# Kernel optimization log

Measured on AMD Instinct MI355X. Metric: run time of the kernel, lower is better.

The kernel has to match this reference:

```python
import jax, jax.numpy as jnp
import numpy as np

THRESH = 0.9   # config['thresh_cnn']
R = 2          # config['radius'] -> maxpool kernel 2R+1=5, stride 1, padding R


def setup_inputs() -> dict:
    key = jax.random.key(0)
    # [B=1, C=1, D=64, H=512, W=512]
    pred_vol = jax.random.uniform(key, (1, 1, 64, 512, 512), dtype=jnp.float32)
    return {"pred_vol": pred_vol}


def reference(pred_vol):
    # threshold: keep values > thresh, else 0
    pred_thresh = jnp.where(pred_vol > THRESH, pred_vol, 0.0)
    # 3D max-pool, kernel 2R+1, stride 1, padding R (torch pads with -inf for maxpool)
    k = 2 * R + 1
    mp = jax.lax.reduce_window(
        pred_thresh, -jnp.inf, jax.lax.max,
        window_dimensions=(1, 1, k, k, k),
        window_strides=(1, 1, 1, 1, 1),
        padding=[(0, 0), (0, 0), (R, R), (R, R), (R, R)],
    )
    # keep only strict local maxima of the thresholded volume
    conf_vol = jnp.where((mp > 0.0) & (mp == pred_thresh), mp, 0.0)
    return jnp.squeeze(conf_vol)  # [D, H, W] dense peak confidence map
```

## Files before the change

### kernel.cpp

```cpp
#include <hip/hip_runtime.h>


#define THRESH 0.9f

constexpr int D = 64, H = 512, W = 512;
constexpr int HW = H * W;
constexpr int TW = 64;
constexpr int TH = 16;
constexpr int DCHUNK = 16;
constexpr int HALO = 2;
constexpr int LROWS = TH + 2 * HALO;
constexpr int WMC = 16;
constexpr int WM_S = WMC + 1;
constexpr int CEN_S = 17;
constexpr int NS = DCHUNK + 2 * HALO;

typedef float floatx4 __attribute__((ext_vector_type(4)));

__device__ __forceinline__ void barrier_no_drain() {
    asm volatile("s_waitcnt lgkmcnt(0)\n\ts_barrier" ::: "memory");
}

__device__ __forceinline__ float4 max4(float4 a, float4 b) {
    return make_float4(fmaxf(a.x, b.x), fmaxf(a.y, b.y),
                       fmaxf(a.z, b.z), fmaxf(a.w, b.w));
}

__device__ __forceinline__ float4 wmax5(float4 a, float4 b, float4 c) {
    const float f2 = a.z, f3 = a.w, f4 = b.x, f5 = b.y, f6 = b.z, f7 = b.w;
    const float f8 = c.x, f9 = c.y;
    const float m45 = fmaxf(f4, f5);
    const float m56 = fmaxf(f5, f6);
    const float m345 = fmaxf(f3, m45);
    const float m456 = fmaxf(f4, m56);
    const float m567 = fmaxf(m56, f7);
    const float m678 = fmaxf(fmaxf(f6, f7), f8);
    float4 r;
    r.x = fmaxf(fmaxf(f2, f6), m345);
    r.y = fmaxf(fmaxf(f3, f7), m456);
    r.z = fmaxf(fmaxf(f4, f8), m567);
    r.w = fmaxf(fmaxf(f5, f9), m678);
    return r;
}

__global__ __launch_bounds__(256)
void peak3d_kernel(const float* __restrict__ in, float* __restrict__ out) {
    __shared__ float4 wm [2][LROWS * WM_S];
    __shared__ float4 cen[2][TH * CEN_S];

    const int tx = threadIdx.x;
    const int ty = threadIdx.y;
    const int tid = ty * 16 + tx;

    const int w0 = blockIdx.x * TW;
    const int h0 = blockIdx.y * TH;
    const int d0 = blockIdx.z * DCHUNK;

    const int rA = tid >> 4, cA = (tid & 15) + 1;
    const bool hasB = (tid < 64);
    const int rB = 16 + (tid >> 4);
    const int cB = cA;

    const int ghA = h0 + rA - HALO;
    const int ghB = h0 + rB - HALO;
    const bool vAr_ = (unsigned)ghA < (unsigned)H;
    const bool vBr_ = hasB && ((unsigned)ghB < (unsigned)H);
    const int gwl = w0 + 4 * cA - 8;
    const int gwm = w0 + 4 * cA - 4;
    const int gwr = w0 + 4 * cA;
    const bool vl = (unsigned)gwl < (unsigned)W;
    const bool vr = (unsigned)gwr < (unsigned)W;
    const size_t offAl = (size_t)(vAr_ ? ghA : 0) * W + (vl ? gwl : 0);
    const size_t offAm = (size_t)(vAr_ ? ghA : 0) * W + gwm;
    const size_t offAr = (size_t)(vAr_ ? ghA : 0) * W + (vr ? gwr : 0);
    const size_t offBl = (size_t)(vBr_ ? ghB : 0) * W + (vl ? gwl : 0);
    const size_t offBm = (size_t)(vBr_ ? ghB : 0) * W + gwm;
    const size_t offBr = (size_t)(vBr_ ? ghB : 0) * W + (vr ? gwr : 0);
    const bool vAl = vAr_ && vl, vAm = vAr_, vArr = vAr_ && vr;
    const bool vBl = vBr_ && vl, vBm = vBr_, vBrr = vBr_ && vr;

    const float4 zero4 = make_float4(0.f, 0.f, 0.f, 0.f);
    float4 win[5], cen_r[3];
#pragma unroll
    for (int k = 0; k < 5; ++k) win[k] = zero4;
#pragma unroll
    for (int k = 0; k < 3; ++k) cen_r[k] = zero4;

    auto ld4 = [&](size_t off) {
        return *reinterpret_cast<const float4*>(in + off);
    };
    auto loadStage = [&](int dd, float4* pf) {
#pragma unroll
        for (int i = 0; i < 6; ++i) pf[i] = zero4;
        if (dd >= 0 && dd < D) {
            const size_t sb = (size_t)dd * HW;
            if (vAl)  pf[0] = ld4(sb + offAl);
            if (vAm)  pf[1] = ld4(sb + offAm);
            if (vArr) pf[2] = ld4(sb + offAr);
            if (vBl)  pf[3] = ld4(sb + offBl);
            if (vBm)  pf[4] = ld4(sb + offBm);
            if (vBrr) pf[5] = ld4(sb + offBr);
        }
    };

    float4 pf[6];
    loadStage(d0 - HALO, pf);

#pragma unroll
    for (int t = 0; t < NS; ++t) {
        const int buf = t & 1;

        {
            const float4 wA = wmax5(pf[0], pf[1], pf[2]);
            wm[buf][rA * WM_S + (cA - 1)] = wA;
            if (rA >= HALO)
                cen[buf][(rA - HALO) * CEN_S + (cA - 1)] = pf[1];
            if (hasB) {
                const float4 wB = wmax5(pf[3], pf[4], pf[5]);
                wm[buf][rB * WM_S + (cB - 1)] = wB;
                if (rB <= TH + HALO - 1)
                    cen[buf][(rB - HALO) * CEN_S + (cB - 1)] = pf[4];
            }
        }
        if (t + 1 < NS) loadStage(d0 - HALO + t + 1, pf);

        barrier_no_drain();

        {
            const float4* wp = &wm[buf][ty * WM_S + tx];
            const float4 hv = max4(max4(max4(wp[0 * WM_S], wp[1 * WM_S]),
                                        max4(wp[3 * WM_S], wp[4 * WM_S])),
                                   wp[2 * WM_S]);
            win[t % 5] = hv;
            cen_r[t % 3] = cen[buf][ty * CEN_S + tx];
        }

        if (t >= 4) {
            const int dout = d0 + (t - 4);
            const float4 mp = max4(max4(max4(win[0], win[1]),
                                        max4(win[2], win[3])), win[4]);
            const float4 c = cen_r[(t + 1) % 3];
            floatx4 res;
            res.x = (c.x > THRESH && mp.x == c.x) ? c.x : 0.f;
            res.y = (c.y > THRESH && mp.y == c.y) ? c.y : 0.f;
            res.z = (c.z > THRESH && mp.z == c.z) ? c.z : 0.f;
            res.w = (c.w > THRESH && mp.w == c.w) ? c.w : 0.f;
            floatx4* op = reinterpret_cast<floatx4*>(
                out + (size_t)dout * HW + (size_t)(h0 + ty) * W + (w0 + 4 * tx));
            __builtin_nontemporal_store(res, op);
        }
    }
}

extern "C" void kernel_launch(void* const* d_in, const int* in_sizes, int n_in,
                              void* d_out, int out_size, void* d_ws, size_t ws_size,
                              hipStream_t stream) {
    const float* in = (const float*)d_in[0];
    float* out = (float*)d_out;
    dim3 grid(W / TW, H / TH, D / DCHUNK);
    dim3 block(16, 16, 1);
    hipLaunchKernelGGL(peak3d_kernel, grid, block, 0, stream, in, out);
}
```

Measured before the change: 117.0 us.

## Use 320-thread blocks with one halo row per thread and halve depth chunk

```diff
diff --git a/kernel.cpp b/kernel.cpp
--- a/kernel.cpp
+++ b/kernel.cpp
@@ -7,11 +7,10 @@
 constexpr int HW = H * W;
 constexpr int TW = 64;
 constexpr int TH = 16;
-constexpr int DCHUNK = 16;
+constexpr int DCHUNK = 8;
 constexpr int HALO = 2;
 constexpr int LROWS = TH + 2 * HALO;
-constexpr int WMC = 16;
-constexpr int WM_S = WMC + 1;
+constexpr int WM_S = 17;
 constexpr int CEN_S = 17;
 constexpr int NS = DCHUNK + 2 * HALO;
 
@@ -43,41 +42,29 @@
     return r;
 }
 
-__global__ __launch_bounds__(256)
+__global__ __launch_bounds__(320, 8)
 void peak3d_kernel(const float* __restrict__ in, float* __restrict__ out) {
     __shared__ float4 wm [2][LROWS * WM_S];
     __shared__ float4 cen[2][TH * CEN_S];
 
     const int tx = threadIdx.x;
     const int ty = threadIdx.y;
-    const int tid = ty * 16 + tx;
 
     const int w0 = blockIdx.x * TW;
     const int h0 = blockIdx.y * TH;
     const int d0 = blockIdx.z * DCHUNK;
 
-    const int rA = tid >> 4, cA = (tid & 15) + 1;
-    const bool hasB = (tid < 64);
-    const int rB = 16 + (tid >> 4);
-    const int cB = cA;
-
-    const int ghA = h0 + rA - HALO;
-    const int ghB = h0 + rB - HALO;
-    const bool vAr_ = (unsigned)ghA < (unsigned)H;
-    const bool vBr_ = hasB && ((unsigned)ghB < (unsigned)H);
-    const int gwl = w0 + 4 * cA - 8;
-    const int gwm = w0 + 4 * cA - 4;
-    const int gwr = w0 + 4 * cA;
-    const bool vl = (unsigned)gwl < (unsigned)W;
-    const bool vr = (unsigned)gwr < (unsigned)W;
-    const size_t offAl = (size_t)(vAr_ ? ghA : 0) * W + (vl ? gwl : 0);
-    const size_t offAm = (size_t)(vAr_ ? ghA : 0) * W + gwm;
-    const size_t offAr = (size_t)(vAr_ ? ghA : 0) * W + (vr ? gwr : 0);
-    const size_t offBl = (size_t)(vBr_ ? ghB : 0) * W + (vl ? gwl : 0);
-    const size_t offBm = (size_t)(vBr_ ? ghB : 0) * W + gwm;
-    const size_t offBr = (size_t)(vBr_ ? ghB : 0) * W + (vr ? gwr : 0);
-    const bool vAl = vAr_ && vl, vAm = vAr_, vArr = vAr_ && vr;
-    const bool vBl = vBr_ && vl, vBm = vBr_, vBrr = vBr_ && vr;
+    const int gh  = h0 + ty - HALO;
+    const bool vR = (unsigned)gh < (unsigned)H;
+    const int gwl = w0 + 4 * tx - 4;
+    const int gwm = w0 + 4 * tx;
+    const int gwr = w0 + 4 * tx + 4;
+    const bool vl = vR && (gwl >= 0);
+    const bool vr = vR && (gwr < W);
+    const size_t rbase = (size_t)(vR ? gh : 0) * W;
+    const size_t offl = rbase + (gwl >= 0 ? gwl : 0);
+    const size_t offm = rbase + gwm;
+    const size_t offr = rbase + (gwr < W ? gwr : 0);
 
     const float4 zero4 = make_float4(0.f, 0.f, 0.f, 0.f);
     float4 win[5], cen_r[3];
@@ -90,64 +77,53 @@
         return *reinterpret_cast<const float4*>(in + off);
     };
     auto loadStage = [&](int dd, float4* pf) {
-#pragma unroll
-        for (int i = 0; i < 6; ++i) pf[i] = zero4;
+        pf[0] = zero4; pf[1] = zero4; pf[2] = zero4;
         if (dd >= 0 && dd < D) {
             const size_t sb = (size_t)dd * HW;
-            if (vAl)  pf[0] = ld4(sb + offAl);
-            if (vAm)  pf[1] = ld4(sb + offAm);
-            if (vArr) pf[2] = ld4(sb + offAr);
-            if (vBl)  pf[3] = ld4(sb + offBl);
-            if (vBm)  pf[4] = ld4(sb + offBm);
-            if (vBrr) pf[5] = ld4(sb + offBr);
+            if (vl) pf[0] = ld4(sb + offl);
+            if (vR) pf[1] = ld4(sb + offm);
+            if (vr) pf[2] = ld4(sb + offr);
         }
     };
 
-    float4 pf[6];
+    float4 pf[3];
     loadStage(d0 - HALO, pf);
 
 #pragma unroll
     for (int t = 0; t < NS; ++t) {
         const int buf = t & 1;
 
-        {
-            const float4 wA = wmax5(pf[0], pf[1], pf[2]);
-            wm[buf][rA * WM_S + (cA - 1)] = wA;
-            if (rA >= HALO)
-                cen[buf][(rA - HALO) * CEN_S + (cA - 1)] = pf[1];
-            if (hasB) {
-                const float4 wB = wmax5(pf[3], pf[4], pf[5]);
-                wm[buf][rB * WM_S + (cB - 1)] = wB;
-                if (rB <= TH + HALO - 1)
-                    cen[buf][(rB - HALO) * CEN_S + (cB - 1)] = pf[4];
-            }
-        }
+        wm[buf][ty * WM_S + tx] = wmax5(pf[0], pf[1], pf[2]);
+        if (ty >= HALO && ty < TH + HALO)
+            cen[buf][(ty - HALO) * CEN_S + tx] = pf[1];
+
         if (t + 1 < NS) loadStage(d0 - HALO + t + 1, pf);
 
         barrier_no_drain();
 
-        {
+        if (ty < TH) {
             const float4* wp = &wm[buf][ty * WM_S + tx];
             const float4 hv = max4(max4(max4(wp[0 * WM_S], wp[1 * WM_S]),
                                         max4(wp[3 * WM_S], wp[4 * WM_S])),
                                    wp[2 * WM_S]);
             win[t % 5] = hv;
             cen_r[t % 3] = cen[buf][ty * CEN_S + tx];
-        }
 
-        if (t >= 4) {
-            const int dout = d0 + (t - 4);
-            const float4 mp = max4(max4(max4(win[0], win[1]),
-                                        max4(win[2], win[3])), win[4]);
-            const float4 c = cen_r[(t + 1) % 3];
-            floatx4 res;
-            res.x = (c.x > THRESH && mp.x == c.x) ? c.x : 0.f;
-            res.y = (c.y > THRESH && mp.y == c.y) ? c.y : 0.f;
-            res.z = (c.z > THRESH && mp.z == c.z) ? c.z : 0.f;
-            res.w = (c.w > THRESH && mp.w == c.w) ? c.w : 0.f;
-            floatx4* op = reinterpret_cast<floatx4*>(
-                out + (size_t)dout * HW + (size_t)(h0 + ty) * W + (w0 + 4 * tx));
-            __builtin_nontemporal_store(res, op);
+            if (t >= 4) {
+                const int dout = d0 + (t - 4);
+                const float4 mp = max4(max4(max4(win[0], win[1]),
+                                            max4(win[2], win[3])), win[4]);
+                const float4 c = cen_r[(t + 1) % 3];
+                floatx4 res;
+                res.x = (c.x > THRESH && mp.x == c.x) ? c.x : 0.f;
+                res.y = (c.y > THRESH && mp.y == c.y) ? c.y : 0.f;
+                res.z = (c.z > THRESH && mp.z == c.z) ? c.z : 0.f;
+                res.w = (c.w > THRESH && mp.w == c.w) ? c.w : 0.f;
+                floatx4* op = reinterpret_cast<floatx4*>(
+                    out + (size_t)dout * HW + (size_t)(h0 + ty) * W +
+                    (w0 + 4 * tx));
+                __builtin_nontemporal_store(res, op);
+            }
         }
     }
 }
@@ -158,6 +134,6 @@
     const float* in = (const float*)d_in[0];
     float* out = (float*)d_out;
     dim3 grid(W / TW, H / TH, D / DCHUNK);
-    dim3 block(16, 16, 1);
+    dim3 block(16, LROWS, 1);
     hipLaunchKernelGGL(peak3d_kernel, grid, block, 0, stream, in, out);
 }
```

Result: slower. 181.6 us (+55.2%).
